# Performance work log

Measured on AMD Instinct MI355X. Metric: run time of the kernel, lower is better.

Reference implementation:

```python
import jax, jax.numpy as jnp
import numpy as np

E, TOP_K, H, I = 8, 2, 1024, 2048
B, S = 1, 2048


def setup_inputs() -> dict:
    key = jax.random.key(0)
    ks = jax.random.split(key, 5)
    scale_h = 1.0 / np.sqrt(H)
    scale_i = 1.0 / np.sqrt(I)
    return {
        "hidden_states": jax.random.normal(ks[0], (B, S, H), dtype=jnp.float32),
        "gate_w": jax.random.normal(ks[1], (E, H), dtype=jnp.float32) * scale_h,
        "w1": jax.random.normal(ks[2], (E, I, H), dtype=jnp.float32) * scale_h,
        "w3": jax.random.normal(ks[3], (E, I, H), dtype=jnp.float32) * scale_h,
        "w2": jax.random.normal(ks[4], (E, H, I), dtype=jnp.float32) * scale_i,
    }


def _moe(x, gate_w, w1, w3, w2):
    orig_shape = x.shape
    xt = x.reshape(-1, H)                       # [T, H]
    logits = xt @ gate_w.T                      # [T, E] router logits
    probs = jax.nn.softmax(logits, axis=-1)
    topw, topi = jax.lax.top_k(probs, TOP_K)    # [T, K]
    topw = topw / jnp.sum(topw, axis=-1, keepdims=True)  # renormalize=True
    # dense per-token expert weights [T, E]
    ew = jnp.sum(jax.nn.one_hot(topi, E, dtype=xt.dtype) * topw[..., None], axis=1)
    # SwiGLU experts, vectorized over all experts
    g = jnp.einsum('th,eih->tei', xt, w1)       # [T, E, I]
    u = jnp.einsum('th,eih->tei', xt, w3)
    act = jax.nn.silu(g) * u
    ye = jnp.einsum('tei,ehi->teh', act, w2)    # [T, E, H]
    out = jnp.einsum('te,teh->th', ew, ye)      # weighted combine
    return out.reshape(orig_shape)


def reference(hidden_states, gate_w, w1, w3, w2):
    return _moe(hidden_states, gate_w, w1, w3, w2)
```

## Files before the change

### kernel.cpp

```cpp
#include <hip/hip_runtime.h>
#include <hip/hip_bf16.h>
#include <math.h>

#define T_TOK 2048
#define HD 1024
#define ID 2048
#define NE 8

typedef __attribute__((ext_vector_type(8))) short s16x8;
typedef __attribute__((ext_vector_type(8))) unsigned short u16x8;
typedef __attribute__((ext_vector_type(4))) float f32x4;
typedef __attribute__((ext_vector_type(4))) unsigned short u16x4;

__device__ __forceinline__ unsigned short f2bf(float f) {
  union { float f; unsigned u; } v; v.f = f;
  unsigned r = v.u + 0x7FFFu + ((v.u >> 16) & 1u);
  return (unsigned short)(r >> 16);
}

__global__ void conv_k(const float* __restrict__ src, unsigned short* __restrict__ dst,
                       int nchunk) {
  int stride = gridDim.x * blockDim.x;
  for (int c = blockIdx.x * blockDim.x + threadIdx.x; c < nchunk; c += stride) {
    const float4* s = (const float4*)(src + (size_t)c * 8);
    float4 f0 = s[0], f1 = s[1];
    u16x8 o;
    o[0] = f2bf(f0.x); o[1] = f2bf(f0.y); o[2] = f2bf(f0.z); o[3] = f2bf(f0.w);
    o[4] = f2bf(f1.x); o[5] = f2bf(f1.y); o[6] = f2bf(f1.z); o[7] = f2bf(f1.w);
    *(u16x8*)(dst + (size_t)c * 8) = o;
  }
}

__global__ void router_k(const float* __restrict__ x, const float* __restrict__ gate,
                         int* __restrict__ cnt, int* __restrict__ tok,
                         float* __restrict__ wt, int* __restrict__ inv) {
  int wid = threadIdx.x >> 6, lane = threadIdx.x & 63;
  int t = blockIdx.x * 4 + wid;
  const float* xr = x + (size_t)t * HD;
  float acc[NE];
#pragma unroll
  for (int e = 0; e < NE; e++) acc[e] = 0.f;
  for (int h = lane; h < HD; h += 64) {
    float xv = xr[h];
#pragma unroll
    for (int e = 0; e < NE; e++) acc[e] += xv * gate[e * HD + h];
  }
#pragma unroll
  for (int e = 0; e < NE; e++)
    for (int off = 32; off; off >>= 1) acc[e] += __shfl_xor(acc[e], off);
  int i0 = 0;
#pragma unroll
  for (int e = 1; e < NE; e++) if (acc[e] > acc[i0]) i0 = e;
  int i1 = (i0 == 0) ? 1 : 0;
#pragma unroll
  for (int e = 0; e < NE; e++) if (e != i0 && acc[e] > acc[i1]) i1 = e;
  float w0 = 1.f / (1.f + expf(acc[i1] - acc[i0]));
  float w1 = 1.f - w0;
  if (lane == 0) {
    int p0 = atomicAdd(&cnt[i0], 1);
    tok[i0 * T_TOK + p0] = t; wt[i0 * T_TOK + p0] = w0;
    inv[2 * t] = (i0 << 16) | p0;
    int p1 = atomicAdd(&cnt[i1], 1);
    tok[i1 * T_TOK + p1] = t; wt[i1 * T_TOK + p1] = w1;
    inv[2 * t + 1] = (i1 << 16) | p1;
  }
}

__global__ void prefix_k(const int* __restrict__ cnt, int* __restrict__ offs) {
  if (threadIdx.x == 0) {
    int s = 0;
    for (int e = 0; e < NE; e++) { offs[e] = s; s += cnt[e]; }
  }
}

__global__ void gather_k(const float* __restrict__ x, const int* __restrict__ cnt,
                         const int* __restrict__ offs, const int* __restrict__ tok,
                         unsigned short* __restrict__ Xg) {
  int e = blockIdx.x >> 11, slot = blockIdx.x & 2047;
  if (slot >= cnt[e]) return;
  int t = tok[e * T_TOK + slot];
  int row = offs[e] + slot;
  int c = threadIdx.x * 4;
  float4 f = *(const float4*)(x + (size_t)t * HD + c);
  u16x4 o; o.x = f2bf(f.x); o.y = f2bf(f.y); o.z = f2bf(f.z); o.w = f2bf(f.w);
  *(u16x4*)(Xg + (size_t)row * HD + c) = o;
}

#define LDT 72

__device__ __forceinline__ void lgkm_barrier() {
  asm volatile("s_waitcnt lgkmcnt(0)" ::: "memory");
  __builtin_amdgcn_s_barrier();
}

__global__ __launch_bounds__(512) void gemm1_k(
    const unsigned short* __restrict__ Xg, const unsigned short* __restrict__ w1b,
    const unsigned short* __restrict__ w3b, const int* __restrict__ cnt,
    const int* __restrict__ offs, const float* __restrict__ wt,
    unsigned short* __restrict__ act) {
  int e = blockIdx.z;
  int count = cnt[e];
  int mt = blockIdx.y;
  if (mt * 128 >= count) return;
  int i0 = blockIdx.x * 128;
  int rbase = offs[e] + mt * 128;
  const unsigned short* W1 = w1b + (size_t)e * ID * HD;
  const unsigned short* W3 = w3b + (size_t)e * ID * HD;

  __shared__ __align__(16) unsigned short As[128 * LDT];
  __shared__ __align__(16) unsigned short B1s[128 * LDT];
  __shared__ __align__(16) unsigned short B2s[128 * LDT];

  int tid = threadIdx.x;
  int ar = tid >> 3, ac = (tid & 7) * 8;
  int wid = tid >> 6, lane = tid & 63;
  int wr = wid >> 2, wc = wid & 3;
  int l15 = lane & 15, lk = (lane >> 4) * 8;

  const unsigned short* aS0 = Xg + (size_t)(rbase + ar) * HD + ac;
  const unsigned short* aS1 = aS0 + (size_t)64 * HD;
  const unsigned short* b1S0 = W1 + (size_t)(i0 + ar) * HD + ac;
  const unsigned short* b1S1 = b1S0 + (size_t)64 * HD;
  const unsigned short* b2S0 = W3 + (size_t)(i0 + ar) * HD + ac;
  const unsigned short* b2S1 = b2S0 + (size_t)64 * HD;
  unsigned short* aD0 = &As[ar * LDT + ac];
  unsigned short* aD1 = aD0 + 64 * LDT;
  unsigned short* b1D0 = &B1s[ar * LDT + ac];
  unsigned short* b1D1 = b1D0 + 64 * LDT;
  unsigned short* b2D0 = &B2s[ar * LDT + ac];
  unsigned short* b2D1 = b2D0 + 64 * LDT;

  f32x4 accg[4][2], accu[4][2];
#pragma unroll
  for (int m = 0; m < 4; m++)
#pragma unroll
    for (int n = 0; n < 2; n++) {
      accg[m][n] = (f32x4){0.f, 0.f, 0.f, 0.f};
      accu[m][n] = (f32x4){0.f, 0.f, 0.f, 0.f};
    }

  u16x8 ra0 = *(const u16x8*)aS0, ra1 = *(const u16x8*)aS1;
  u16x8 r10 = *(const u16x8*)b1S0, r11 = *(const u16x8*)b1S1;
  u16x8 r20 = *(const u16x8*)b2S0, r21 = *(const u16x8*)b2S1;

  for (int t = 0; t < 16; ++t) {
    lgkm_barrier();
    *(u16x8*)aD0 = ra0;  *(u16x8*)aD1 = ra1;
    *(u16x8*)b1D0 = r10; *(u16x8*)b1D1 = r11;
    *(u16x8*)b2D0 = r20; *(u16x8*)b2D1 = r21;
    lgkm_barrier();
    if (t < 15) {
      int k0 = (t + 1) * 64;
      ra0 = *(const u16x8*)(aS0 + k0);  ra1 = *(const u16x8*)(aS1 + k0);
      r10 = *(const u16x8*)(b1S0 + k0); r11 = *(const u16x8*)(b1S1 + k0);
      r20 = *(const u16x8*)(b2S0 + k0); r21 = *(const u16x8*)(b2S1 + k0);
    }
#pragma unroll
    for (int kk = 0; kk < 2; ++kk) {
      s16x8 a[4], b1[2], b2[2];
#pragma unroll
      for (int m = 0; m < 4; m++)
        a[m] = *(const s16x8*)&As[(wr * 64 + m * 16 + l15) * LDT + kk * 32 + lk];
#pragma unroll
      for (int n = 0; n < 2; n++) {
        b1[n] = *(const s16x8*)&B1s[(wc * 32 + n * 16 + l15) * LDT + kk * 32 + lk];
        b2[n] = *(const s16x8*)&B2s[(wc * 32 + n * 16 + l15) * LDT + kk * 32 + lk];
      }
#pragma unroll
      for (int m = 0; m < 4; m++)
#pragma unroll
        for (int n = 0; n < 2; n++) {
          accg[m][n] = __builtin_amdgcn_mfma_f32_16x16x32_bf16(a[m], b1[n], accg[m][n], 0, 0, 0);
          accu[m][n] = __builtin_amdgcn_mfma_f32_16x16x32_bf16(a[m], b2[n], accu[m][n], 0, 0, 0);
        }
    }
  }

#pragma unroll
  for (int m = 0; m < 4; m++)
#pragma unroll
    for (int r = 0; r < 4; r++) {
      int rl = mt * 128 + wr * 64 + m * 16 + (lane >> 4) * 4 + r;
      if (rl < count) {
        float w = wt[e * T_TOK + rl];
#pragma unroll
        for (int n = 0; n < 2; n++) {
          float g = accg[m][n][r], u = accu[m][n][r];
          float s = (g / (1.f + expf(-g))) * u * w;
          act[(size_t)(offs[e] + rl) * ID + i0 + wc * 32 + n * 16 + l15] = f2bf(s);
        }
      }
    }
}

__global__ __launch_bounds__(256) void gemm2_k(
    const unsigned short* __restrict__ act, const unsigned short* __restrict__ w2b,
    const int* __restrict__ cnt, const int* __restrict__ offs,
    float* __restrict__ ye) {
  int e = blockIdx.z;
  int count = cnt[e];
  int mt = blockIdx.y;
  if (mt * 64 >= count) return;
  int h0 = blockIdx.x * 128;
  int rbase = offs[e] + mt * 64;
  const unsigned short* W2 = w2b + (size_t)e * HD * ID;

  __shared__ __align__(16) unsigned short As[64 * LDT];
  __shared__ __align__(16) unsigned short Bs[128 * LDT];

  int tid = threadIdx.x;
  int ar = tid >> 3, ac = (tid & 7) * 8;
  int wc = tid >> 6, lane = tid & 63;
  int l15 = lane & 15, lk = (lane >> 4) * 8;

  const unsigned short* aS0 = act + (size_t)(rbase + ar) * ID + ac;
  const unsigned short* aS1 = aS0 + (size_t)32 * ID;
  const unsigned short* bS0 = W2 + (size_t)(h0 + ar) * ID + ac;
  const unsigned short* bS1 = bS0 + (size_t)32 * ID;
  const unsigned short* bS2 = bS0 + (size_t)64 * ID;
  const unsigned short* bS3 = bS0 + (size_t)96 * ID;
  unsigned short* aD0 = &As[ar * LDT + ac];
  unsigned short* aD1 = aD0 + 32 * LDT;
  unsigned short* bD0 = &Bs[ar * LDT + ac];
  unsigned short* bD1 = bD0 + 32 * LDT;
  unsigned short* bD2 = bD0 + 64 * LDT;
  unsigned short* bD3 = bD0 + 96 * LDT;

  f32x4 acc[4][2];
#pragma unroll
  for (int m = 0; m < 4; m++)
#pragma unroll
    for (int n = 0; n < 2; n++) acc[m][n] = (f32x4){0.f, 0.f, 0.f, 0.f};

  u16x8 ra0 = *(const u16x8*)aS0, ra1 = *(const u16x8*)aS1;
  u16x8 rb0 = *(const u16x8*)bS0, rb1 = *(const u16x8*)bS1;
  u16x8 rb2 = *(const u16x8*)bS2, rb3 = *(const u16x8*)bS3;

  for (int t = 0; t < 32; ++t) {
    lgkm_barrier();
    *(u16x8*)aD0 = ra0; *(u16x8*)aD1 = ra1;
    *(u16x8*)bD0 = rb0; *(u16x8*)bD1 = rb1;
    *(u16x8*)bD2 = rb2; *(u16x8*)bD3 = rb3;
    lgkm_barrier();
    if (t < 31) {
      int k0 = (t + 1) * 64;
      ra0 = *(const u16x8*)(aS0 + k0); ra1 = *(const u16x8*)(aS1 + k0);
      rb0 = *(const u16x8*)(bS0 + k0); rb1 = *(const u16x8*)(bS1 + k0);
      rb2 = *(const u16x8*)(bS2 + k0); rb3 = *(const u16x8*)(bS3 + k0);
    }
#pragma unroll
    for (int kk = 0; kk < 2; ++kk) {
      s16x8 a[4], b[2];
#pragma unroll
      for (int m = 0; m < 4; m++)
        a[m] = *(const s16x8*)&As[(m * 16 + l15) * LDT + kk * 32 + lk];
#pragma unroll
      for (int n = 0; n < 2; n++)
        b[n] = *(const s16x8*)&Bs[(wc * 32 + n * 16 + l15) * LDT + kk * 32 + lk];
#pragma unroll
      for (int m = 0; m < 4; m++)
#pragma unroll
        for (int n = 0; n < 2; n++)
          acc[m][n] = __builtin_amdgcn_mfma_f32_16x16x32_bf16(a[m], b[n], acc[m][n], 0, 0, 0);
    }
  }

#pragma unroll
  for (int m = 0; m < 4; m++)
#pragma unroll
    for (int r = 0; r < 4; r++) {
      int slot = mt * 64 + m * 16 + (lane >> 4) * 4 + r;
      if (slot < count) {
#pragma unroll
        for (int n = 0; n < 2; n++)
          ye[(size_t)(offs[e] + slot) * HD + h0 + wc * 32 + n * 16 + l15] = acc[m][n][r];
      }
    }
}

__global__ void combine_k(const float* __restrict__ ye, const int* __restrict__ inv,
                          const int* __restrict__ offs, float* __restrict__ out) {
  int t = blockIdx.x;
  int c = threadIdx.x * 4;
  int v0 = inv[2 * t], v1 = inv[2 * t + 1];
  int r0 = offs[v0 >> 16] + (v0 & 0xFFFF);
  int r1 = offs[v1 >> 16] + (v1 & 0xFFFF);
  float4 a = *(const float4*)(ye + (size_t)r0 * HD + c);
  float4 b = *(const float4*)(ye + (size_t)r1 * HD + c);
  float4 o = {a.x + b.x, a.y + b.y, a.z + b.z, a.w + b.w};
  *(float4*)(out + (size_t)t * HD + c) = o;
}

extern "C" void kernel_launch(void* const* d_in, const int* in_sizes, int n_in,
                              void* d_out, int out_size, void* d_ws, size_t ws_size,
                              hipStream_t stream) {
  const float* x    = (const float*)d_in[0];
  const float* gate = (const float*)d_in[1];
  const float* w1   = (const float*)d_in[2];
  const float* w3   = (const float*)d_in[3];
  const float* w2   = (const float*)d_in[4];
  float* out = (float*)d_out;

  char* ws = (char*)d_ws;
  int* cnt  = (int*)(ws + 0);
  int* offs = (int*)(ws + 256);
  int* tok  = (int*)(ws + 512);
  float* wt = (float*)(ws + 66048);
  int* inv  = (int*)(ws + 131584);
  unsigned short* Xg  = (unsigned short*)(ws + 148480);
  unsigned short* act = (unsigned short*)(ws + 8799232);
  float* ye = (float*)(ws + 26100736);
  unsigned short* w1b = (unsigned short*)(ws + 43402240);
  unsigned short* w3b = (unsigned short*)(ws + 76956672);
  unsigned short* w2b = (unsigned short*)(ws + 110511104);

  hipMemsetAsync(cnt, 0, 256, stream);

  const int WCHUNK = (NE * ID * HD) / 8;
  conv_k<<<2048, 256, 0, stream>>>(w1, w1b, WCHUNK);
  conv_k<<<2048, 256, 0, stream>>>(w3, w3b, WCHUNK);
  conv_k<<<2048, 256, 0, stream>>>(w2, w2b, WCHUNK);

  router_k<<<T_TOK / 4, 256, 0, stream>>>(x, gate, cnt, tok, wt, inv);
  prefix_k<<<1, 64, 0, stream>>>(cnt, offs);
  gather_k<<<NE * T_TOK, 256, 0, stream>>>(x, cnt, offs, tok, Xg);
  gemm1_k<<<dim3(ID / 128, 16, NE), 512, 0, stream>>>(Xg, w1b, w3b, cnt, offs, wt, act);
  gemm2_k<<<dim3(HD / 128, 32, NE), 256, 0, stream>>>(act, w2b, cnt, offs, ye);
  combine_k<<<T_TOK, 256, 0, stream>>>(ye, inv, offs, out);
}
```

Baseline: 409.8 us.

## Fuse weight bf16 conversion into GEMM loads and stream activations via LDS DMA

```diff
diff --git a/kernel.cpp b/kernel.cpp
--- a/kernel.cpp
+++ b/kernel.cpp
@@ -6,6 +6,7 @@
 #define HD 1024
 #define ID 2048
 #define NE 8
+#define LDT 72
 
 typedef __attribute__((ext_vector_type(8))) short s16x8;
 typedef __attribute__((ext_vector_type(8))) unsigned short u16x8;
@@ -18,18 +19,21 @@
   return (unsigned short)(r >> 16);
 }
 
-__global__ void conv_k(const float* __restrict__ src, unsigned short* __restrict__ dst,
-                       int nchunk) {
-  int stride = gridDim.x * blockDim.x;
-  for (int c = blockIdx.x * blockDim.x + threadIdx.x; c < nchunk; c += stride) {
-    const float4* s = (const float4*)(src + (size_t)c * 8);
-    float4 f0 = s[0], f1 = s[1];
-    u16x8 o;
-    o[0] = f2bf(f0.x); o[1] = f2bf(f0.y); o[2] = f2bf(f0.z); o[3] = f2bf(f0.w);
-    o[4] = f2bf(f1.x); o[5] = f2bf(f1.y); o[6] = f2bf(f1.z); o[7] = f2bf(f1.w);
-    *(u16x8*)(dst + (size_t)c * 8) = o;
-  }
-}
+__device__ __forceinline__ u16x8 pack8(float4 a, float4 b) {
+  u16x8 v;
+  v[0] = f2bf(a.x); v[1] = f2bf(a.y); v[2] = f2bf(a.z); v[3] = f2bf(a.w);
+  v[4] = f2bf(b.x); v[5] = f2bf(b.y); v[6] = f2bf(b.z); v[7] = f2bf(b.w);
+  return v;
+}
+
+__device__ __forceinline__ void lgkm_barrier() {
+  asm volatile("s_waitcnt lgkmcnt(0)" ::: "memory");
+  __builtin_amdgcn_s_barrier();
+}
+
+#define GLOAD16(gsrc, ldst) \
+  __builtin_amdgcn_global_load_lds((const __attribute__((address_space(1))) void*)(gsrc), \
+                                   (__attribute__((address_space(3))) void*)(ldst), 16, 0, 0)
 
 __global__ void router_k(const float* __restrict__ x, const float* __restrict__ gate,
                          int* __restrict__ cnt, int* __restrict__ tok,
@@ -86,49 +90,38 @@
   *(u16x4*)(Xg + (size_t)row * HD + c) = o;
 }
 
-#define LDT 72
-
-__device__ __forceinline__ void lgkm_barrier() {
-  asm volatile("s_waitcnt lgkmcnt(0)" ::: "memory");
-  __builtin_amdgcn_s_barrier();
-}
-
-__global__ __launch_bounds__(512) void gemm1_k(
-    const unsigned short* __restrict__ Xg, const unsigned short* __restrict__ w1b,
-    const unsigned short* __restrict__ w3b, const int* __restrict__ cnt,
+__global__ __launch_bounds__(256, 3) void gemm1_k(
+    const unsigned short* __restrict__ Xg, const float* __restrict__ w1,
+    const float* __restrict__ w3, const int* __restrict__ cnt,
     const int* __restrict__ offs, const float* __restrict__ wt,
     unsigned short* __restrict__ act) {
   int e = blockIdx.z;
   int count = cnt[e];
   int mt = blockIdx.y;
   if (mt * 128 >= count) return;
-  int i0 = blockIdx.x * 128;
+  int i0 = blockIdx.x * 64;
   int rbase = offs[e] + mt * 128;
-  const unsigned short* W1 = w1b + (size_t)e * ID * HD;
-  const unsigned short* W3 = w3b + (size_t)e * ID * HD;
-
-  __shared__ __align__(16) unsigned short As[128 * LDT];
-  __shared__ __align__(16) unsigned short B1s[128 * LDT];
-  __shared__ __align__(16) unsigned short B2s[128 * LDT];
+  const float* W1 = w1 + (size_t)e * ID * HD;
+  const float* W3 = w3 + (size_t)e * ID * HD;
+
+  __shared__ __align__(16) unsigned short Abuf[2][128 * 64];
+  __shared__ __align__(16) unsigned short B1s[64 * LDT];
+  __shared__ __align__(16) unsigned short B2s[64 * LDT];
 
   int tid = threadIdx.x;
-  int ar = tid >> 3, ac = (tid & 7) * 8;
   int wid = tid >> 6, lane = tid & 63;
-  int wr = wid >> 2, wc = wid & 3;
-  int l15 = lane & 15, lk = (lane >> 4) * 8;
-
-  const unsigned short* aS0 = Xg + (size_t)(rbase + ar) * HD + ac;
-  const unsigned short* aS1 = aS0 + (size_t)64 * HD;
-  const unsigned short* b1S0 = W1 + (size_t)(i0 + ar) * HD + ac;
-  const unsigned short* b1S1 = b1S0 + (size_t)64 * HD;
-  const unsigned short* b2S0 = W3 + (size_t)(i0 + ar) * HD + ac;
-  const unsigned short* b2S1 = b2S0 + (size_t)64 * HD;
-  unsigned short* aD0 = &As[ar * LDT + ac];
-  unsigned short* aD1 = aD0 + 64 * LDT;
-  unsigned short* b1D0 = &B1s[ar * LDT + ac];
-  unsigned short* b1D1 = b1D0 + 64 * LDT;
-  unsigned short* b2D0 = &B2s[ar * LDT + ac];
-  unsigned short* b2D1 = b2D0 + 64 * LDT;
+  int wr = wid >> 1, wc = wid & 1;
+  int l15 = lane & 15, hi = lane >> 4;
+  int br = tid >> 2, bc = (tid & 3) * 16;
+
+  int swz_col = ((lane & 7) ^ (lane >> 3)) * 8;
+  const unsigned short* ag[4];
+#pragma unroll
+  for (int c = 0; c < 4; c++)
+    ag[c] = Xg + (size_t)(rbase + c * 32 + wid * 8 + (lane >> 3)) * HD + swz_col;
+
+  const float* s1 = W1 + (size_t)(i0 + br) * HD + bc;
+  const float* s2 = W3 + (size_t)(i0 + br) * HD + bc;
 
   f32x4 accg[4][2], accu[4][2];
 #pragma unroll
@@ -139,32 +132,44 @@
       accu[m][n] = (f32x4){0.f, 0.f, 0.f, 0.f};
     }
 
-  u16x8 ra0 = *(const u16x8*)aS0, ra1 = *(const u16x8*)aS1;
-  u16x8 r10 = *(const u16x8*)b1S0, r11 = *(const u16x8*)b1S1;
-  u16x8 r20 = *(const u16x8*)b2S0, r21 = *(const u16x8*)b2S1;
+#pragma unroll
+  for (int c = 0; c < 4; c++) GLOAD16(ag[c], &Abuf[0][c * 2048 + wid * 512]);
+  float4 p1[4], p2[4];
+#pragma unroll
+  for (int j = 0; j < 4; j++) { p1[j] = *(const float4*)(s1 + j * 4); p2[j] = *(const float4*)(s2 + j * 4); }
 
   for (int t = 0; t < 16; ++t) {
+    int cur = t & 1;
     lgkm_barrier();
-    *(u16x8*)aD0 = ra0;  *(u16x8*)aD1 = ra1;
-    *(u16x8*)b1D0 = r10; *(u16x8*)b1D1 = r11;
-    *(u16x8*)b2D0 = r20; *(u16x8*)b2D1 = r21;
+    *(u16x8*)&B1s[br * LDT + bc]     = pack8(p1[0], p1[1]);
+    *(u16x8*)&B1s[br * LDT + bc + 8] = pack8(p1[2], p1[3]);
+    *(u16x8*)&B2s[br * LDT + bc]     = pack8(p2[0], p2[1]);
+    *(u16x8*)&B2s[br * LDT + bc + 8] = pack8(p2[2], p2[3]);
     lgkm_barrier();
+    __builtin_amdgcn_sched_barrier(0);
     if (t < 15) {
-      int k0 = (t + 1) * 64;
-      ra0 = *(const u16x8*)(aS0 + k0);  ra1 = *(const u16x8*)(aS1 + k0);
-      r10 = *(const u16x8*)(b1S0 + k0); r11 = *(const u16x8*)(b1S1 + k0);
-      r20 = *(const u16x8*)(b2S0 + k0); r21 = *(const u16x8*)(b2S1 + k0);
+      int k0n = (t + 1) * 64;
+#pragma unroll
+      for (int c = 0; c < 4; c++)
+        GLOAD16(ag[c] + k0n, &Abuf[cur ^ 1][c * 2048 + wid * 512]);
+#pragma unroll
+      for (int j = 0; j < 4; j++) {
+        p1[j] = *(const float4*)(s1 + k0n + j * 4);
+        p2[j] = *(const float4*)(s2 + k0n + j * 4);
+      }
     }
 #pragma unroll
     for (int kk = 0; kk < 2; ++kk) {
       s16x8 a[4], b1[2], b2[2];
 #pragma unroll
-      for (int m = 0; m < 4; m++)
-        a[m] = *(const s16x8*)&As[(wr * 64 + m * 16 + l15) * LDT + kk * 32 + lk];
+      for (int m = 0; m < 4; m++) {
+        int r = wr * 64 + m * 16 + l15;
+        a[m] = *(const s16x8*)&Abuf[cur][r * 64 + (((kk * 4 + hi) ^ (r & 7)) * 8)];
+      }
 #pragma unroll
       for (int n = 0; n < 2; n++) {
-        b1[n] = *(const s16x8*)&B1s[(wc * 32 + n * 16 + l15) * LDT + kk * 32 + lk];
-        b2[n] = *(const s16x8*)&B2s[(wc * 32 + n * 16 + l15) * LDT + kk * 32 + lk];
+        b1[n] = *(const s16x8*)&B1s[(wc * 32 + n * 16 + l15) * LDT + kk * 32 + hi * 8];
+        b2[n] = *(const s16x8*)&B2s[(wc * 32 + n * 16 + l15) * LDT + kk * 32 + hi * 8];
       }
 #pragma unroll
       for (int m = 0; m < 4; m++)
@@ -193,38 +198,34 @@
     }
 }
 
-__global__ __launch_bounds__(256) void gemm2_k(
-    const unsigned short* __restrict__ act, const unsigned short* __restrict__ w2b,
+__global__ __launch_bounds__(256, 3) void gemm2_k(
+    const unsigned short* __restrict__ act, const float* __restrict__ w2,
     const int* __restrict__ cnt, const int* __restrict__ offs,
     float* __restrict__ ye) {
   int e = blockIdx.z;
   int count = cnt[e];
   int mt = blockIdx.y;
-  if (mt * 64 >= count) return;
-  int h0 = blockIdx.x * 128;
-  int rbase = offs[e] + mt * 64;
-  const unsigned short* W2 = w2b + (size_t)e * HD * ID;
-
-  __shared__ __align__(16) unsigned short As[64 * LDT];
-  __shared__ __align__(16) unsigned short Bs[128 * LDT];
+  if (mt * 128 >= count) return;
+  int h0 = blockIdx.x * 64;
+  int rbase = offs[e] + mt * 128;
+  const float* W2 = w2 + (size_t)e * HD * ID;
+
+  __shared__ __align__(16) unsigned short Abuf[2][128 * 64];
+  __shared__ __align__(16) unsigned short Bs[64 * LDT];
 
   int tid = threadIdx.x;
-  int ar = tid >> 3, ac = (tid & 7) * 8;
-  int wc = tid >> 6, lane = tid & 63;
-  int l15 = lane & 15, lk = (lane >> 4) * 8;
-
-  const unsigned short* aS0 = act + (size_t)(rbase + ar) * ID + ac;
-  const unsigned short* aS1 = aS0 + (size_t)32 * ID;
-  const unsigned short* bS0 = W2 + (size_t)(h0 + ar) * ID + ac;
-  const unsigned short* bS1 = bS0 + (size_t)32 * ID;
-  const unsigned short* bS2 = bS0 + (size_t)64 * ID;
-  const unsigned short* bS3 = bS0 + (size_t)96 * ID;
-  unsigned short* aD0 = &As[ar * LDT + ac];
-  unsigned short* aD1 = aD0 + 32 * LDT;
-  unsigned short* bD0 = &Bs[ar * LDT + ac];
-  unsigned short* bD1 = bD0 + 32 * LDT;
-  unsigned short* bD2 = bD0 + 64 * LDT;
-  unsigned short* bD3 = bD0 + 96 * LDT;
+  int wid = tid >> 6, lane = tid & 63;
+  int wr = wid >> 1, wc = wid & 1;
+  int l15 = lane & 15, hi = lane >> 4;
+  int br = tid >> 2, bc = (tid & 3) * 16;
+
+  int swz_col = ((lane & 7) ^ (lane >> 3)) * 8;
+  const unsigned short* ag[4];
+#pragma unroll
+  for (int c = 0; c < 4; c++)
+    ag[c] = act + (size_t)(rbase + c * 32 + wid * 8 + (lane >> 3)) * ID + swz_col;
+
+  const float* sb = W2 + (size_t)(h0 + br) * ID + bc;
 
   f32x4 acc[4][2];
 #pragma unroll
@@ -232,31 +233,38 @@
 #pragma unroll
     for (int n = 0; n < 2; n++) acc[m][n] = (f32x4){0.f, 0.f, 0.f, 0.f};
 
-  u16x8 ra0 = *(const u16x8*)aS0, ra1 = *(const u16x8*)aS1;
-  u16x8 rb0 = *(const u16x8*)bS0, rb1 = *(const u16x8*)bS1;
-  u16x8 rb2 = *(const u16x8*)bS2, rb3 = *(const u16x8*)bS3;
+#pragma unroll
+  for (int c = 0; c < 4; c++) GLOAD16(ag[c], &Abuf[0][c * 2048 + wid * 512]);
+  float4 pb[4];
+#pragma unroll
+  for (int j = 0; j < 4; j++) pb[j] = *(const float4*)(sb + j * 4);
 
   for (int t = 0; t < 32; ++t) {
+    int cur = t & 1;
     lgkm_barrier();
-    *(u16x8*)aD0 = ra0; *(u16x8*)aD1 = ra1;
-    *(u16x8*)bD0 = rb0; *(u16x8*)bD1 = rb1;
-    *(u16x8*)bD2 = rb2; *(u16x8*)bD3 = rb3;
+    *(u16x8*)&Bs[br * LDT + bc]     = pack8(pb[0], pb[1]);
+    *(u16x8*)&Bs[br * LDT + bc + 8] = pack8(pb[2], pb[3]);
     lgkm_barrier();
+    __builtin_amdgcn_sched_barrier(0);
     if (t < 31) {
-      int k0 = (t + 1) * 64;
-      ra0 = *(const u16x8*)(aS0 + k0); ra1 = *(const u16x8*)(aS1 + k0);
-      rb0 = *(const u16x8*)(bS0 + k0); rb1 = *(const u16x8*)(bS1 + k0);
-      rb2 = *(const u16x8*)(bS2 + k0); rb3 = *(const u16x8*)(bS3 + k0);
+      int k0n = (t + 1) * 64;
+#pragma unroll
+      for (int c = 0; c < 4; c++)
+        GLOAD16(ag[c] + k0n, &Abuf[cur ^ 1][c * 2048 + wid * 512]);
+#pragma unroll
+      for (int j = 0; j < 4; j++) pb[j] = *(const float4*)(sb + k0n + j * 4);
     }
 #pragma unroll
     for (int kk = 0; kk < 2; ++kk) {
       s16x8 a[4], b[2];
 #pragma unroll
-      for (int m = 0; m < 4; m++)
-        a[m] = *(const s16x8*)&As[(m * 16 + l15) * LDT + kk * 32 + lk];
+      for (int m = 0; m < 4; m++) {
+        int r = wr * 64 + m * 16 + l15;
+        a[m] = *(const s16x8*)&Abuf[cur][r * 64 + (((kk * 4 + hi) ^ (r & 7)) * 8)];
+      }
 #pragma unroll
       for (int n = 0; n < 2; n++)
-        b[n] = *(const s16x8*)&Bs[(wc * 32 + n * 16 + l15) * LDT + kk * 32 + lk];
+        b[n] = *(const s16x8*)&Bs[(wc * 32 + n * 16 + l15) * LDT + kk * 32 + hi * 8];
 #pragma unroll
       for (int m = 0; m < 4; m++)
 #pragma unroll
@@ -269,7 +277,7 @@
   for (int m = 0; m < 4; m++)
 #pragma unroll
     for (int r = 0; r < 4; r++) {
-      int slot = mt * 64 + m * 16 + (lane >> 4) * 4 + r;
+      int slot = mt * 128 + wr * 64 + m * 16 + (lane >> 4) * 4 + r;
       if (slot < count) {
 #pragma unroll
         for (int n = 0; n < 2; n++)
@@ -310,21 +318,13 @@
   unsigned short* Xg  = (unsigned short*)(ws + 148480);
   unsigned short* act = (unsigned short*)(ws + 8799232);
   float* ye = (float*)(ws + 26100736);
-  unsigned short* w1b = (unsigned short*)(ws + 43402240);
-  unsigned short* w3b = (unsigned short*)(ws + 76956672);
-  unsigned short* w2b = (unsigned short*)(ws + 110511104);
 
   hipMemsetAsync(cnt, 0, 256, stream);
-
-  const int WCHUNK = (NE * ID * HD) / 8;
-  conv_k<<<2048, 256, 0, stream>>>(w1, w1b, WCHUNK);
-  conv_k<<<2048, 256, 0, stream>>>(w3, w3b, WCHUNK);
-  conv_k<<<2048, 256, 0, stream>>>(w2, w2b, WCHUNK);
 
   router_k<<<T_TOK / 4, 256, 0, stream>>>(x, gate, cnt, tok, wt, inv);
   prefix_k<<<1, 64, 0, stream>>>(cnt, offs);
   gather_k<<<NE * T_TOK, 256, 0, stream>>>(x, cnt, offs, tok, Xg);
-  gemm1_k<<<dim3(ID / 128, 16, NE), 512, 0, stream>>>(Xg, w1b, w3b, cnt, offs, wt, act);
-  gemm2_k<<<dim3(HD / 128, 32, NE), 256, 0, stream>>>(act, w2b, cnt, offs, ye);
+  gemm1_k<<<dim3(ID / 64, 16, NE), 256, 0, stream>>>(Xg, w1, w3, cnt, offs, wt, act);
+  gemm2_k<<<dim3(HD / 64, 16, NE), 256, 0, stream>>>(act, w2, cnt, offs, ye);
   combine_k<<<T_TOK, 256, 0, stream>>>(ye, inv, offs, out);
 }
```

Result: faster. 371.1 us (-9.5%).
